# Kernel optimization log

Measured on AMD Instinct MI355X. Metric: run time of the kernel, lower is better.

Reference implementation:

```python
import jax, jax.numpy as jnp
import numpy as np

B, S, D = 2, 2048, 512
H, HD = 8, 64  # num_heads, head_size; all_head_size = H*HD = 512


def setup_inputs() -> dict:
    key = jax.random.key(0)
    ks = jax.random.split(key, 11)
    sc = 0.02
    return {
        "query": jax.random.normal(ks[0], (B, S, D), jnp.float32),
        "key": jax.random.normal(ks[1], (B, S, D), jnp.float32),
        "value": jax.random.normal(ks[2], (B, S, D), jnp.float32),
        "Wq": jax.random.normal(ks[3], (D, H * HD), jnp.float32) * sc,
        "bq": jnp.zeros((H * HD,), jnp.float32),
        "Wk": jax.random.normal(ks[4], (D, H * HD), jnp.float32) * sc,
        "bk": jnp.zeros((H * HD,), jnp.float32),
        "Wv": jax.random.normal(ks[5], (D, H * HD), jnp.float32) * sc,
        "bv": jnp.zeros((H * HD,), jnp.float32),
        "Wo": jax.random.normal(ks[6], (H * HD, D), jnp.float32) * sc,
        "bo": jnp.zeros((D,), jnp.float32),
    }


def _split_heads(x):
    b, s, _ = x.shape
    return x.reshape(b, s, H, HD).transpose(0, 2, 1, 3)  # [B,H,S,HD]


def reference(query, key, value, Wq, bq, Wk, bk, Wv, bv, Wo, bo):
    q = _split_heads(query @ Wq + bq)
    k = _split_heads(key @ Wk + bk)
    v = _split_heads(value @ Wv + bv)
    scores = jnp.einsum("bhqd,bhkd->bhqk", q, k) / jnp.sqrt(jnp.asarray(HD, q.dtype))
    probs = jax.nn.softmax(scores, axis=-1)  # dropout rate 0.0, inference
    ctx = jnp.einsum("bhqk,bhkd->bhqd", probs, v)
    ctx = ctx.transpose(0, 2, 1, 3).reshape(query.shape[0], -1, H * HD)
    return ctx @ Wo + bo
```

## Files before the change

kernel.cpp:

```cpp
#include <hip/hip_runtime.h>
#include <math.h>

#define BATCH 2
#define SEQ 2048
#define DMODEL 512
#define NH 8
#define HDIM 64
#define MTOT (BATCH * SEQ)
#define QSIZE (BATCH * NH * SEQ * HDIM)
#define WSIZE (DMODEL * DMODEL)

typedef __attribute__((ext_vector_type(8))) short bf16x8;
typedef __attribute__((ext_vector_type(4))) float f32x4;

__device__ inline unsigned short f2bf(float f) {
    union { float f; unsigned u; } v; v.f = f;
    unsigned u = v.u;
    u += 0x7fffu + ((u >> 16) & 1u);
    return (unsigned short)(u >> 16);
}
__device__ inline unsigned pack2(float lo, float hi) {
    unsigned r;
    asm("v_cvt_pk_bf16_f32 %0, %1, %2" : "=v"(r) : "v"(lo), "v"(hi));
    return r;
}

#define LSTR 72

#define WS_Q   ((size_t)0)
#define WS_K   ((size_t)QSIZE)
#define WS_V   (2 * (size_t)QSIZE)
#define WS_CTX (3 * (size_t)QSIZE)
#define WS_WT  (4 * (size_t)QSIZE)
#define WS_ABF (4 * (size_t)QSIZE + 4 * (size_t)WSIZE)

__global__ __launch_bounds__(256) void wt_prep_kernel(
    const float* __restrict__ Wq, const float* __restrict__ Wk,
    const float* __restrict__ Wv, const float* __restrict__ Wo,
    unsigned short* __restrict__ wt)
{
    const int z = blockIdx.z;
    const float* W = (z == 0) ? Wq : (z == 1) ? Wk : (z == 2) ? Wv : Wo;
    unsigned short* Wt = wt + (size_t)z * WSIZE;

    __shared__ float T[32][33];
    const int tid = threadIdx.x;
    const int k0 = blockIdx.x * 32, n0 = blockIdx.y * 32;

    {
        int r = tid >> 3, c = (tid & 7) * 4;
        float4 v = *(const float4*)&W[(size_t)(k0 + r) * DMODEL + n0 + c];
        T[r][c + 0] = v.x; T[r][c + 1] = v.y; T[r][c + 2] = v.z; T[r][c + 3] = v.w;
    }
    __syncthreads();
    {
        int n = tid >> 3, c = (tid & 7) * 4;
        uint2 o;
        o.x = pack2(T[c + 0][n], T[c + 1][n]);
        o.y = pack2(T[c + 2][n], T[c + 3][n]);
        *(uint2*)&Wt[(size_t)(n0 + n) * DMODEL + k0 + c] = o;
    }
}

__global__ __launch_bounds__(256) void inp_prep_kernel(
    const float* __restrict__ qin, const float* __restrict__ kin,
    const float* __restrict__ vin, unsigned short* __restrict__ abf)
{
    const int z = blockIdx.y;
    const float* src = (z == 0) ? qin : (z == 1) ? kin : vin;
    unsigned short* dst = abf + (size_t)z * QSIZE;

    const size_t i = ((size_t)blockIdx.x * 256 + threadIdx.x) * 8;
    float4 f0 = *(const float4*)(src + i);
    float4 f1 = *(const float4*)(src + i + 4);
    uint4 o;
    o.x = pack2(f0.x, f0.y); o.y = pack2(f0.z, f0.w);
    o.z = pack2(f1.x, f1.y); o.w = pack2(f1.z, f1.w);
    *(uint4*)(dst + i) = o;
}

__global__ __launch_bounds__(256) void qkv_mfma_kernel(
    unsigned short* __restrict__ ws,
    const float* __restrict__ bq, const float* __restrict__ bk,
    const float* __restrict__ bv)
{
    const int which = blockIdx.z;
    const unsigned short* A  = ws + WS_ABF + (size_t)which * QSIZE;
    const unsigned short* Wt = ws + WS_WT + (size_t)which * WSIZE;
    const float* bias = (which == 0) ? bq : (which == 1) ? bk : bv;
    unsigned short* out = ws + (size_t)which * QSIZE;

    __shared__ __align__(16) short As[128][LSTR];
    __shared__ __align__(16) short Bs[128][LSTR];

    const int tid = threadIdx.x;
    const int lane = tid & 63, wave = tid >> 6;
    const int lrow = lane & 15, quad = lane >> 4;
    const int m0 = blockIdx.y * 128, n0 = blockIdx.x * 128;

    const int sr = tid >> 1;
    const int sh = (tid & 1) * 32;

    f32x4 acc[2][8];
    #pragma unroll
    for (int i = 0; i < 2; ++i)
        #pragma unroll
        for (int n = 0; n < 8; ++n) acc[i][n] = f32x4{0.f, 0.f, 0.f, 0.f};

    for (int k0 = 0; k0 < DMODEL; k0 += 64) {
        __syncthreads();
        {
            const unsigned short* ap = A + (size_t)(m0 + sr) * DMODEL + k0 + sh;
            uint4 a0 = *(const uint4*)(ap + 0),  a1 = *(const uint4*)(ap + 8);
            uint4 a2 = *(const uint4*)(ap + 16), a3 = *(const uint4*)(ap + 24);
            *(uint4*)&As[sr][sh + 0]  = a0;
            *(uint4*)&As[sr][sh + 8]  = a1;
            *(uint4*)&As[sr][sh + 16] = a2;
            *(uint4*)&As[sr][sh + 24] = a3;
        }
        {
            const unsigned short* wp = Wt + (size_t)(n0 + sr) * DMODEL + k0 + sh;
            uint4 b0 = *(const uint4*)(wp + 0),  b1 = *(const uint4*)(wp + 8);
            uint4 b2 = *(const uint4*)(wp + 16), b3 = *(const uint4*)(wp + 24);
            *(uint4*)&Bs[sr][sh + 0]  = b0;
            *(uint4*)&Bs[sr][sh + 8]  = b1;
            *(uint4*)&Bs[sr][sh + 16] = b2;
            *(uint4*)&Bs[sr][sh + 24] = b3;
        }
        __syncthreads();
        #pragma unroll
        for (int s = 0; s < 2; ++s) {
            bf16x8 af[2];
            #pragma unroll
            for (int i = 0; i < 2; ++i)
                af[i] = *(const bf16x8*)&As[wave * 32 + i * 16 + lrow][s * 32 + quad * 8];
            #pragma unroll
            for (int n = 0; n < 8; ++n) {
                bf16x8 bf = *(const bf16x8*)&Bs[n * 16 + lrow][s * 32 + quad * 8];
                acc[0][n] = __builtin_amdgcn_mfma_f32_16x16x32_bf16(af[0], bf, acc[0][n], 0, 0, 0);
                acc[1][n] = __builtin_amdgcn_mfma_f32_16x16x32_bf16(af[1], bf, acc[1][n], 0, 0, 0);
            }
        }
    }

    if (which < 2) {
        const float scale = (which == 0) ? 0.125f : 1.0f;
        #pragma unroll
        for (int n = 0; n < 8; ++n) {
            const int col = n0 + n * 16 + lrow;
            const int h_ = col >> 6, hd_ = col & 63;
            const float bv_ = bias[col];
            #pragma unroll
            for (int i = 0; i < 2; ++i) {
                #pragma unroll
                for (int r = 0; r < 4; ++r) {
                    const int m = m0 + wave * 32 + i * 16 + quad * 4 + r;
                    const int b_ = m >> 11, s_ = m & (SEQ - 1);
                    const float v = (acc[i][n][r] + bv_) * scale;
                    out[((size_t)((b_ * NH + h_) * SEQ + s_)) * HDIM + hd_] = f2bf(v);
                }
            }
        }
    } else {
        #pragma unroll
        for (int n = 0; n < 8; ++n) {
            const int col = n0 + n * 16 + lrow;
            const int h_ = col >> 6, hd_ = col & 63;
            const float bv_ = bias[col];
            #pragma unroll
            for (int i = 0; i < 2; ++i) {
                const int m = m0 + wave * 32 + i * 16 + quad * 4;
                const int b_ = m >> 11, s_ = m & (SEQ - 1);
                uint2 o;
                o.x = pack2(acc[i][n][0] + bv_, acc[i][n][1] + bv_);
                o.y = pack2(acc[i][n][2] + bv_, acc[i][n][3] + bv_);
                *(uint2*)&out[((size_t)((b_ * NH + h_) * HDIM + hd_)) * SEQ + s_] = o;
            }
        }
    }
}

#define HSEQ (SEQ / 2)
#define NT   (HSEQ / 64)
#define OSTR 68

__global__ __launch_bounds__(512) void attn_mfma_kernel(
    const unsigned short* __restrict__ ws, unsigned short* __restrict__ ctx)
{
    const unsigned short* Q = ws + WS_Q;
    const unsigned short* K = ws + WS_K;
    const unsigned short* V = ws + WS_V;

    __shared__ __align__(16) short Ks[2][2][64][LSTR];
    __shared__ __align__(16) short Vt[2][2][64][LSTR];

    const int lin = blockIdx.x + 16 * blockIdx.y;
    const int bh  = (lin & 7) + 8 * (lin >> 8);
    const int q0  = ((lin >> 3) & 31) * 64;

    const int tid = threadIdx.x;
    const int lane = tid & 63, wave = tid >> 6;
    const int half = wave >> 2, w4 = wave & 3;
    const int lrow = lane & 15, quad = lane >> 4;
    const size_t base = (size_t)bh * SEQ * HDIM;

    const unsigned short* qrow = Q + base + (size_t)(q0 + w4 * 16 + lrow) * HDIM;
    const bf16x8 qb0 = *(const bf16x8*)(qrow + quad * 8);
    const bf16x8 qb1 = *(const bf16x8*)(qrow + 32 + quad * 8);

    float m_prev = -1e30f, l_run = 0.f;
    f32x4 oacc[4];
    #pragma unroll
    for (int n = 0; n < 4; ++n) oacc[n] = f32x4{0.f, 0.f, 0.f, 0.f};

    const int t  = tid & 255;
    const int kr = t >> 2;
    const int kc = (t & 3) * 16;
    const int n_ = t & 3;
    const int c0 = ((n_ >= 2) ? 32 : 0) + (n_ & 1) * 4;
    const int ktbase = half * HSEQ;

    const unsigned short* kptr = K + base + (size_t)(ktbase + kr) * HDIM + kc;
    const unsigned short* vptr = V + base + (size_t)kr * SEQ + ktbase + kc;

    uint4 kA, kB, vA, vB;
#define LOADT(TI) do { \
        const unsigned short* kp = kptr + (size_t)(TI) * 64 * HDIM; \
        const unsigned short* vp = vptr + (TI) * 64; \
        kA = *(const uint4*)kp; kB = *(const uint4*)(kp + 8); \
        vA = *(const uint4*)vp; vB = *(const uint4*)(vp + 8); \
    } while (0)
#define WRITET(BUF) do { \
        *(uint4*)&Ks[half][BUF][kr][kc]     = kA; \
        *(uint4*)&Ks[half][BUF][kr][kc + 8] = kB; \
        uint2 w0; w0.x = vA.x; w0.y = vA.y; \
        uint2 w1; w1.x = vA.z; w1.y = vA.w; \
        uint2 w2; w2.x = vB.x; w2.y = vB.y; \
        uint2 w3; w3.x = vB.z; w3.y = vB.w; \
        *(uint2*)&Vt[half][BUF][kr][c0]      = w0; \
        *(uint2*)&Vt[half][BUF][kr][c0 + 8]  = w1; \
        *(uint2*)&Vt[half][BUF][kr][c0 + 16] = w2; \
        *(uint2*)&Vt[half][BUF][kr][c0 + 24] = w3; \
    } while (0)

    LOADT(0);
    WRITET(0);
    LOADT(1);

    #pragma unroll 2
    for (int ti = 0; ti < NT; ++ti) {
        const int cur = ti & 1;
        __syncthreads();

        f32x4 st[4];
        __builtin_amdgcn_s_setprio(1);
        #pragma unroll
        for (int n = 0; n < 4; ++n) {
            bf16x8 ka0 = *(const bf16x8*)&Ks[half][cur][n * 16 + lrow][quad * 8];
            bf16x8 ka1 = *(const bf16x8*)&Ks[half][cur][n * 16 + lrow][32 + quad * 8];
            f32x4 z = f32x4{0.f, 0.f, 0.f, 0.f};
            z = __builtin_amdgcn_mfma_f32_16x16x32_bf16(ka0, qb0, z, 0, 0, 0);
            z = __builtin_amdgcn_mfma_f32_16x16x32_bf16(ka1, qb1, z, 0, 0, 0);
            st[n] = z;
        }
        __builtin_amdgcn_s_setprio(0);

        float tmax = st[0][0];
        #pragma unroll
        for (int n = 0; n < 4; ++n)
            #pragma unroll
            for (int r = 0; r < 4; ++r) tmax = fmaxf(tmax, st[n][r]);
        tmax = fmaxf(tmax, __shfl_xor(tmax, 16));
        tmax = fmaxf(tmax, __shfl_xor(tmax, 32));

        if (!__all(tmax <= m_prev + 8.f)) {
            const float mnew = fmaxf(m_prev, tmax);
            const float alpha = __expf(m_prev - mnew);
            l_run *= alpha;
            #pragma unroll
            for (int n = 0; n < 4; ++n) {
                oacc[n][0] *= alpha; oacc[n][1] *= alpha;
                oacc[n][2] *= alpha; oacc[n][3] *= alpha;
            }
            m_prev = mnew;
        }

        float p[4][4];
        float tsum = 0.f;
        #pragma unroll
        for (int n = 0; n < 4; ++n)
            #pragma unroll
            for (int r = 0; r < 4; ++r) {
                p[n][r] = __expf(st[n][r] - m_prev);
                tsum += p[n][r];
            }
        tsum += __shfl_xor(tsum, 16);
        tsum += __shfl_xor(tsum, 32);
        l_run += tsum;

        union { unsigned w[4]; bf16x8 v; } U0, U1;
        U0.w[0] = pack2(p[0][0], p[0][1]); U0.w[1] = pack2(p[0][2], p[0][3]);
        U0.w[2] = pack2(p[1][0], p[1][1]); U0.w[3] = pack2(p[1][2], p[1][3]);
        U1.w[0] = pack2(p[2][0], p[2][1]); U1.w[1] = pack2(p[2][2], p[2][3]);
        U1.w[2] = pack2(p[3][0], p[3][1]); U1.w[3] = pack2(p[3][2], p[3][3]);

        __builtin_amdgcn_s_setprio(1);
        #pragma unroll
        for (int n = 0; n < 4; ++n) {
            bf16x8 va0 = *(const bf16x8*)&Vt[half][cur][n * 16 + lrow][quad * 8];
            bf16x8 va1 = *(const bf16x8*)&Vt[half][cur][n * 16 + lrow][32 + quad * 8];
            oacc[n] = __builtin_amdgcn_mfma_f32_16x16x32_bf16(va0, U0.v, oacc[n], 0, 0, 0);
            oacc[n] = __builtin_amdgcn_mfma_f32_16x16x32_bf16(va1, U1.v, oacc[n], 0, 0, 0);
        }
        __builtin_amdgcn_s_setprio(0);

        if (ti < NT - 1) WRITET(cur ^ 1);
        if (ti < NT - 2) LOADT(ti + 2);
    }
#undef LOADT
#undef WRITET

    __syncthreads();
    float* Obuf = (float*)&Ks[0][0][0][0];
    float* Mbuf = (float*)&Vt[0][0][0][0];

    if (half == 1) {
        float* ob = Obuf + (size_t)w4 * (16 * OSTR) + (size_t)lrow * OSTR;
        #pragma unroll
        for (int n = 0; n < 4; ++n)
            *(f32x4*)&ob[n * 16 + quad * 4] = oacc[n];
        if (quad == 0) {
            Mbuf[w4 * 16 + lrow]      = m_prev;
            Mbuf[64 + w4 * 16 + lrow] = l_run;
        }
    }
    __syncthreads();
    if (half == 0) {
        const float m1 = Mbuf[w4 * 16 + lrow];
        const float l1 = Mbuf[64 + w4 * 16 + lrow];
        const float M  = fmaxf(m_prev, m1);
        const float a0 = __expf(m_prev - M), a1 = __expf(m1 - M);
        const float inv = 1.f / (l_run * a0 + l1 * a1);
        const float s0 = a0 * inv, s1 = a1 * inv;
        const float* ob = Obuf + (size_t)w4 * (16 * OSTR) + (size_t)lrow * OSTR;

        const int b_ = bh >> 3, h_ = bh & 7;
        const int qg = q0 + w4 * 16 + lrow;
        unsigned short* crow = ctx + ((size_t)(b_ * SEQ + qg)) * DMODEL + h_ * HDIM;
        #pragma unroll
        for (int n = 0; n < 4; ++n) {
            f32x4 o1 = *(const f32x4*)&ob[n * 16 + quad * 4];
            uint2 o;
            o.x = pack2(oacc[n][0] * s0 + o1[0] * s1, oacc[n][1] * s0 + o1[1] * s1);
            o.y = pack2(oacc[n][2] * s0 + o1[2] * s1, oacc[n][3] * s0 + o1[3] * s1);
            *(uint2*)&crow[n * 16 + quad * 4] = o;
        }
    }
}

__global__ __launch_bounds__(256) void out_proj_mfma_kernel(
    const unsigned short* __restrict__ ws, const float* __restrict__ bo,
    float* __restrict__ out)
{
    const unsigned short* ctx = ws + WS_CTX;
    const unsigned short* Wt  = ws + WS_WT + 3 * (size_t)WSIZE;

    __shared__ __align__(16) short As[128][LSTR];
    __shared__ __align__(16) short Bs[64][LSTR];

    const int tid = threadIdx.x;
    const int lane = tid & 63, wave = tid >> 6;
    const int lrow = lane & 15, quad = lane >> 4;
    const int m0 = blockIdx.y * 128, n0 = blockIdx.x * 64;

    const int sr = tid >> 1, sh = (tid & 1) * 32;
    const int br = tid >> 2, bqr = (tid & 3) * 16;

    f32x4 acc[2][4];
    #pragma unroll
    for (int i = 0; i < 2; ++i)
        #pragma unroll
        for (int n = 0; n < 4; ++n) acc[i][n] = f32x4{0.f, 0.f, 0.f, 0.f};

    for (int k0 = 0; k0 < DMODEL; k0 += 64) {
        __syncthreads();
        {
            const unsigned short* ap = ctx + (size_t)(m0 + sr) * DMODEL + k0 + sh;
            uint4 c0 = *(const uint4*)(ap + 0),  c1 = *(const uint4*)(ap + 8);
            uint4 c2 = *(const uint4*)(ap + 16), c3 = *(const uint4*)(ap + 24);
            *(uint4*)&As[sr][sh + 0]  = c0;
            *(uint4*)&As[sr][sh + 8]  = c1;
            *(uint4*)&As[sr][sh + 16] = c2;
            *(uint4*)&As[sr][sh + 24] = c3;
        }
        {
            const unsigned short* wp = Wt + (size_t)(n0 + br) * DMODEL + k0 + bqr;
            uint4 b0 = *(const uint4*)wp;
            uint4 b1 = *(const uint4*)(wp + 8);
            *(uint4*)&Bs[br][bqr]     = b0;
            *(uint4*)&Bs[br][bqr + 8] = b1;
        }
        __syncthreads();
        #pragma unroll
        for (int s = 0; s < 2; ++s) {
            bf16x8 af[2];
            #pragma unroll
            for (int i = 0; i < 2; ++i)
                af[i] = *(const bf16x8*)&As[wave * 32 + i * 16 + lrow][s * 32 + quad * 8];
            #pragma unroll
            for (int n = 0; n < 4; ++n) {
                bf16x8 bf = *(const bf16x8*)&Bs[n * 16 + lrow][s * 32 + quad * 8];
                acc[0][n] = __builtin_amdgcn_mfma_f32_16x16x32_bf16(af[0], bf, acc[0][n], 0, 0, 0);
                acc[1][n] = __builtin_amdgcn_mfma_f32_16x16x32_bf16(af[1], bf, acc[1][n], 0, 0, 0);
            }
        }
    }

    #pragma unroll
    for (int n = 0; n < 4; ++n) {
        const int col = n0 + n * 16 + lrow;
        const float bv_ = bo[col];
        #pragma unroll
        for (int i = 0; i < 2; ++i) {
            #pragma unroll
            for (int r = 0; r < 4; ++r) {
                const int m = m0 + wave * 32 + i * 16 + quad * 4 + r;
                out[(size_t)m * DMODEL + col] = acc[i][n][r] + bv_;
            }
        }
    }
}

extern "C" void kernel_launch(void* const* d_in, const int* in_sizes, int n_in,
                              void* d_out, int out_size, void* d_ws, size_t ws_size,
                              hipStream_t stream)
{
    const float* qin = (const float*)d_in[0];
    const float* kin = (const float*)d_in[1];
    const float* vin = (const float*)d_in[2];
    const float* Wq  = (const float*)d_in[3];
    const float* bq  = (const float*)d_in[4];
    const float* Wk  = (const float*)d_in[5];
    const float* bk  = (const float*)d_in[6];
    const float* Wv  = (const float*)d_in[7];
    const float* bv  = (const float*)d_in[8];
    const float* Wo  = (const float*)d_in[9];
    const float* bo  = (const float*)d_in[10];

    unsigned short* ws = (unsigned short*)d_ws;
    float* out = (float*)d_out;

    dim3 gw(DMODEL / 32, DMODEL / 32, 4);
    wt_prep_kernel<<<gw, 256, 0, stream>>>(Wq, Wk, Wv, Wo, ws + WS_WT);

    dim3 gi(QSIZE / (256 * 8), 3);
    inp_prep_kernel<<<gi, 256, 0, stream>>>(qin, kin, vin, ws + WS_ABF);

    dim3 gp(DMODEL / 128, MTOT / 128, 3);
    qkv_mfma_kernel<<<gp, 256, 0, stream>>>(ws, bq, bk, bv);

    dim3 ga(BATCH * NH, SEQ / 64);
    attn_mfma_kernel<<<ga, 512, 0, stream>>>(ws, ws + WS_CTX);

    dim3 go(DMODEL / 64, MTOT / 128);
    out_proj_mfma_kernel<<<go, 256, 0, stream>>>(ws, bo, out);
}
```

Baseline: 147.7 us.

## Fuse input bf16 conversion into QKV GEMM, double-buffer weights, use exp2 softmax

The separate fp32-to-bf16 input prep kernel is removed, and the QKV GEMM now loads fp32 activations straight from global memory into registers, converting them in place. Both projection GEMMs drop the A-tile shared-memory staging and double-buffer the B tile, so each k-step needs one barrier instead of two. Attention folds log2(e) into the Q scale so softmax can use exp2f, raises the lazy-rescale threshold, and does the row-sum shuffle reduction once at the end instead of every tile. The cost is uncoalesced, per-lane global reads of A that are reused from registers rather than shared memory, plus a looser rescale bound that could affect accuracy.

```diff
diff --git a/kernel.cpp b/kernel.cpp
--- a/kernel.cpp
+++ b/kernel.cpp
@@ -32,7 +32,8 @@
 #define WS_V   (2 * (size_t)QSIZE)
 #define WS_CTX (3 * (size_t)QSIZE)
 #define WS_WT  (4 * (size_t)QSIZE)
-#define WS_ABF (4 * (size_t)QSIZE + 4 * (size_t)WSIZE)
+
+#define QSCALE 0.1803368801111204f
 
 __global__ __launch_bounds__(256) void wt_prep_kernel(
     const float* __restrict__ Wq, const float* __restrict__ Wk,
@@ -62,44 +63,31 @@
     }
 }
 
-__global__ __launch_bounds__(256) void inp_prep_kernel(
-    const float* __restrict__ qin, const float* __restrict__ kin,
-    const float* __restrict__ vin, unsigned short* __restrict__ abf)
-{
-    const int z = blockIdx.y;
-    const float* src = (z == 0) ? qin : (z == 1) ? kin : vin;
-    unsigned short* dst = abf + (size_t)z * QSIZE;
-
-    const size_t i = ((size_t)blockIdx.x * 256 + threadIdx.x) * 8;
-    float4 f0 = *(const float4*)(src + i);
-    float4 f1 = *(const float4*)(src + i + 4);
-    uint4 o;
-    o.x = pack2(f0.x, f0.y); o.y = pack2(f0.z, f0.w);
-    o.z = pack2(f1.x, f1.y); o.w = pack2(f1.z, f1.w);
-    *(uint4*)(dst + i) = o;
-}
-
 __global__ __launch_bounds__(256) void qkv_mfma_kernel(
     unsigned short* __restrict__ ws,
+    const float* __restrict__ qin, const float* __restrict__ kin,
+    const float* __restrict__ vin,
     const float* __restrict__ bq, const float* __restrict__ bk,
     const float* __restrict__ bv)
 {
     const int which = blockIdx.z;
-    const unsigned short* A  = ws + WS_ABF + (size_t)which * QSIZE;
+    const float* A = (which == 0) ? qin : (which == 1) ? kin : vin;
     const unsigned short* Wt = ws + WS_WT + (size_t)which * WSIZE;
     const float* bias = (which == 0) ? bq : (which == 1) ? bk : bv;
     unsigned short* out = ws + (size_t)which * QSIZE;
 
-    __shared__ __align__(16) short As[128][LSTR];
-    __shared__ __align__(16) short Bs[128][LSTR];
+    __shared__ __align__(16) short Bs[2][128][LSTR];
 
     const int tid = threadIdx.x;
     const int lane = tid & 63, wave = tid >> 6;
     const int lrow = lane & 15, quad = lane >> 4;
     const int m0 = blockIdx.y * 128, n0 = blockIdx.x * 128;
 
-    const int sr = tid >> 1;
-    const int sh = (tid & 1) * 32;
+    const int sr = tid >> 1, sh = (tid & 1) * 32;
+    const unsigned short* wp0 = Wt + (size_t)(n0 + sr) * DMODEL + sh;
+
+    const float* arow0 = A + (size_t)(m0 + wave * 32 + lrow) * DMODEL;
+    const float* arow1 = arow0 + 16 * DMODEL;
 
     f32x4 acc[2][8];
     #pragma unroll
@@ -107,44 +95,59 @@
         #pragma unroll
         for (int n = 0; n < 8; ++n) acc[i][n] = f32x4{0.f, 0.f, 0.f, 0.f};
 
-    for (int k0 = 0; k0 < DMODEL; k0 += 64) {
+    uint4 b0, b1, b2, b3;
+#define LOADB(K0) do { const unsigned short* wp = wp0 + (K0); \
+        b0 = *(const uint4*)(wp + 0);  b1 = *(const uint4*)(wp + 8); \
+        b2 = *(const uint4*)(wp + 16); b3 = *(const uint4*)(wp + 24); } while (0)
+#define WRITEB(BUF) do { \
+        *(uint4*)&Bs[BUF][sr][sh + 0]  = b0; *(uint4*)&Bs[BUF][sr][sh + 8]  = b1; \
+        *(uint4*)&Bs[BUF][sr][sh + 16] = b2; *(uint4*)&Bs[BUF][sr][sh + 24] = b3; } while (0)
+
+    LOADB(0);
+    WRITEB(0);
+    LOADB(64);
+
+    #pragma unroll
+    for (int kk = 0; kk < 8; ++kk) {
+        const int k0 = kk * 64, cur = kk & 1;
         __syncthreads();
-        {
-            const unsigned short* ap = A + (size_t)(m0 + sr) * DMODEL + k0 + sh;
-            uint4 a0 = *(const uint4*)(ap + 0),  a1 = *(const uint4*)(ap + 8);
-            uint4 a2 = *(const uint4*)(ap + 16), a3 = *(const uint4*)(ap + 24);
-            *(uint4*)&As[sr][sh + 0]  = a0;
-            *(uint4*)&As[sr][sh + 8]  = a1;
-            *(uint4*)&As[sr][sh + 16] = a2;
-            *(uint4*)&As[sr][sh + 24] = a3;
-        }
-        {
-            const unsigned short* wp = Wt + (size_t)(n0 + sr) * DMODEL + k0 + sh;
-            uint4 b0 = *(const uint4*)(wp + 0),  b1 = *(const uint4*)(wp + 8);
-            uint4 b2 = *(const uint4*)(wp + 16), b3 = *(const uint4*)(wp + 24);
-            *(uint4*)&Bs[sr][sh + 0]  = b0;
-            *(uint4*)&Bs[sr][sh + 8]  = b1;
-            *(uint4*)&Bs[sr][sh + 16] = b2;
-            *(uint4*)&Bs[sr][sh + 24] = b3;
-        }
-        __syncthreads();
+        __builtin_amdgcn_s_setprio(1);
         #pragma unroll
         for (int s = 0; s < 2; ++s) {
+            const int cb = k0 + s * 32 + quad * 8;
             bf16x8 af[2];
-            #pragma unroll
-            for (int i = 0; i < 2; ++i)
-                af[i] = *(const bf16x8*)&As[wave * 32 + i * 16 + lrow][s * 32 + quad * 8];
+            {
+                float4 f0 = *(const float4*)(arow0 + cb);
+                float4 f1 = *(const float4*)(arow0 + cb + 4);
+                union { unsigned w[4]; bf16x8 v; } U;
+                U.w[0] = pack2(f0.x, f0.y); U.w[1] = pack2(f0.z, f0.w);
+                U.w[2] = pack2(f1.x, f1.y); U.w[3] = pack2(f1.z, f1.w);
+                af[0] = U.v;
+            }
+            {
+                float4 f0 = *(const float4*)(arow1 + cb);
+                float4 f1 = *(const float4*)(arow1 + cb + 4);
+                union { unsigned w[4]; bf16x8 v; } U;
+                U.w[0] = pack2(f0.x, f0.y); U.w[1] = pack2(f0.z, f0.w);
+                U.w[2] = pack2(f1.x, f1.y); U.w[3] = pack2(f1.z, f1.w);
+                af[1] = U.v;
+            }
             #pragma unroll
             for (int n = 0; n < 8; ++n) {
-                bf16x8 bf = *(const bf16x8*)&Bs[n * 16 + lrow][s * 32 + quad * 8];
-                acc[0][n] = __builtin_amdgcn_mfma_f32_16x16x32_bf16(af[0], bf, acc[0][n], 0, 0, 0);
-                acc[1][n] = __builtin_amdgcn_mfma_f32_16x16x32_bf16(af[1], bf, acc[1][n], 0, 0, 0);
-            }
-        }
-    }
+                bf16x8 bfv = *(const bf16x8*)&Bs[cur][n * 16 + lrow][s * 32 + quad * 8];
+                acc[0][n] = __builtin_amdgcn_mfma_f32_16x16x32_bf16(af[0], bfv, acc[0][n], 0, 0, 0);
+                acc[1][n] = __builtin_amdgcn_mfma_f32_16x16x32_bf16(af[1], bfv, acc[1][n], 0, 0, 0);
+            }
+        }
+        __builtin_amdgcn_s_setprio(0);
+        if (kk < 7) WRITEB(cur ^ 1);
+        if (kk < 6) LOADB(k0 + 128);
+    }
+#undef LOADB
+#undef WRITEB
 
     if (which < 2) {
-        const float scale = (which == 0) ? 0.125f : 1.0f;
+        const float scale = (which == 0) ? QSCALE : 1.0f;
         #pragma unroll
         for (int n = 0; n < 8; ++n) {
             const int col = n0 + n * 16 + lrow;
@@ -183,6 +186,7 @@
 #define HSEQ (SEQ / 2)
 #define NT   (HSEQ / 64)
 #define OSTR 68
+#define THR2 11.0f
 
 __global__ __launch_bounds__(512) void attn_mfma_kernel(
     const unsigned short* __restrict__ ws, unsigned short* __restrict__ ctx)
@@ -265,17 +269,17 @@
         }
         __builtin_amdgcn_s_setprio(0);
 
-        float tmax = st[0][0];
-        #pragma unroll
-        for (int n = 0; n < 4; ++n)
-            #pragma unroll
-            for (int r = 0; r < 4; ++r) tmax = fmaxf(tmax, st[n][r]);
+        float t0 = fmaxf(fmaxf(st[0][0], st[0][1]), fmaxf(st[0][2], st[0][3]));
+        float t1 = fmaxf(fmaxf(st[1][0], st[1][1]), fmaxf(st[1][2], st[1][3]));
+        float t2 = fmaxf(fmaxf(st[2][0], st[2][1]), fmaxf(st[2][2], st[2][3]));
+        float t3 = fmaxf(fmaxf(st[3][0], st[3][1]), fmaxf(st[3][2], st[3][3]));
+        float tmax = fmaxf(fmaxf(t0, t1), fmaxf(t2, t3));
         tmax = fmaxf(tmax, __shfl_xor(tmax, 16));
         tmax = fmaxf(tmax, __shfl_xor(tmax, 32));
 
-        if (!__all(tmax <= m_prev + 8.f)) {
+        if (!__all(tmax <= m_prev + THR2)) {
             const float mnew = fmaxf(m_prev, tmax);
-            const float alpha = __expf(m_prev - mnew);
+            const float alpha = exp2f(m_prev - mnew);
             l_run *= alpha;
             #pragma unroll
             for (int n = 0; n < 4; ++n) {
@@ -291,11 +295,9 @@
         for (int n = 0; n < 4; ++n)
             #pragma unroll
             for (int r = 0; r < 4; ++r) {
-                p[n][r] = __expf(st[n][r] - m_prev);
+                p[n][r] = exp2f(st[n][r] - m_prev);
                 tsum += p[n][r];
             }
-        tsum += __shfl_xor(tsum, 16);
-        tsum += __shfl_xor(tsum, 32);
         l_run += tsum;
 
         union { unsigned w[4]; bf16x8 v; } U0, U1;
@@ -320,6 +322,9 @@
 #undef LOADT
 #undef WRITET
 
+    l_run += __shfl_xor(l_run, 16);
+    l_run += __shfl_xor(l_run, 32);
+
     __syncthreads();
     float* Obuf = (float*)&Ks[0][0][0][0];
     float* Mbuf = (float*)&Vt[0][0][0][0];
@@ -339,7 +344,7 @@
         const float m1 = Mbuf[w4 * 16 + lrow];
         const float l1 = Mbuf[64 + w4 * 16 + lrow];
         const float M  = fmaxf(m_prev, m1);
-        const float a0 = __expf(m_prev - M), a1 = __expf(m1 - M);
+        const float a0 = exp2f(m_prev - M), a1 = exp2f(m1 - M);
         const float inv = 1.f / (l_run * a0 + l1 * a1);
         const float s0 = a0 * inv, s1 = a1 * inv;
         const float* ob = Obuf + (size_t)w4 * (16 * OSTR) + (size_t)lrow * OSTR;
@@ -365,16 +370,18 @@
     const unsigned short* ctx = ws + WS_CTX;
     const unsigned short* Wt  = ws + WS_WT + 3 * (size_t)WSIZE;
 
-    __shared__ __align__(16) short As[128][LSTR];
-    __shared__ __align__(16) short Bs[64][LSTR];
+    __shared__ __align__(16) short Bs[2][64][LSTR];
 
     const int tid = threadIdx.x;
     const int lane = tid & 63, wave = tid >> 6;
     const int lrow = lane & 15, quad = lane >> 4;
     const int m0 = blockIdx.y * 128, n0 = blockIdx.x * 64;
 
-    const int sr = tid >> 1, sh = (tid & 1) * 32;
-    const int br = tid >> 2, bqr = (tid & 3) * 16;
+    const int br = tid >> 2, bc = (tid & 3) * 16;
+    const unsigned short* wp0 = Wt + (size_t)(n0 + br) * DMODEL + bc;
+
+    const unsigned short* arow0 = ctx + (size_t)(m0 + wave * 32 + lrow) * DMODEL;
+    const unsigned short* arow1 = arow0 + 16 * DMODEL;
 
     f32x4 acc[2][4];
     #pragma unroll
@@ -382,39 +389,40 @@
         #pragma unroll
         for (int n = 0; n < 4; ++n) acc[i][n] = f32x4{0.f, 0.f, 0.f, 0.f};
 
-    for (int k0 = 0; k0 < DMODEL; k0 += 64) {
+    uint4 b0, b1;
+#define LOADB(K0) do { const unsigned short* wp = wp0 + (K0); \
+        b0 = *(const uint4*)(wp + 0); b1 = *(const uint4*)(wp + 8); } while (0)
+#define WRITEB(BUF) do { \
+        *(uint4*)&Bs[BUF][br][bc]     = b0; \
+        *(uint4*)&Bs[BUF][br][bc + 8] = b1; } while (0)
+
+    LOADB(0);
+    WRITEB(0);
+    LOADB(64);
+
+    #pragma unroll
+    for (int kk = 0; kk < 8; ++kk) {
+        const int k0 = kk * 64, cur = kk & 1;
         __syncthreads();
-        {
-            const unsigned short* ap = ctx + (size_t)(m0 + sr) * DMODEL + k0 + sh;
-            uint4 c0 = *(const uint4*)(ap + 0),  c1 = *(const uint4*)(ap + 8);
-            uint4 c2 = *(const uint4*)(ap + 16), c3 = *(const uint4*)(ap + 24);
-            *(uint4*)&As[sr][sh + 0]  = c0;
-            *(uint4*)&As[sr][sh + 8]  = c1;
-            *(uint4*)&As[sr][sh + 16] = c2;
-            *(uint4*)&As[sr][sh + 24] = c3;
-        }
-        {
-            const unsigned short* wp = Wt + (size_t)(n0 + br) * DMODEL + k0 + bqr;
-            uint4 b0 = *(const uint4*)wp;
-            uint4 b1 = *(const uint4*)(wp + 8);
-            *(uint4*)&Bs[br][bqr]     = b0;
-            *(uint4*)&Bs[br][bqr + 8] = b1;
-        }
-        __syncthreads();
+        __builtin_amdgcn_s_setprio(1);
         #pragma unroll
         for (int s = 0; s < 2; ++s) {
-            bf16x8 af[2];
-            #pragma unroll
-            for (int i = 0; i < 2; ++i)
-                af[i] = *(const bf16x8*)&As[wave * 32 + i * 16 + lrow][s * 32 + quad * 8];
+            const int cb = k0 + s * 32 + quad * 8;
+            bf16x8 af0 = *(const bf16x8*)(arow0 + cb);
+            bf16x8 af1 = *(const bf16x8*)(arow1 + cb);
             #pragma unroll
             for (int n = 0; n < 4; ++n) {
-                bf16x8 bf = *(const bf16x8*)&Bs[n * 16 + lrow][s * 32 + quad * 8];
-                acc[0][n] = __builtin_amdgcn_mfma_f32_16x16x32_bf16(af[0], bf, acc[0][n], 0, 0, 0);
-                acc[1][n] = __builtin_amdgcn_mfma_f32_16x16x32_bf16(af[1], bf, acc[1][n], 0, 0, 0);
-            }
-        }
-    }
+                bf16x8 bfv = *(const bf16x8*)&Bs[cur][n * 16 + lrow][s * 32 + quad * 8];
+                acc[0][n] = __builtin_amdgcn_mfma_f32_16x16x32_bf16(af0, bfv, acc[0][n], 0, 0, 0);
+                acc[1][n] = __builtin_amdgcn_mfma_f32_16x16x32_bf16(af1, bfv, acc[1][n], 0, 0, 0);
+            }
+        }
+        __builtin_amdgcn_s_setprio(0);
+        if (kk < 7) WRITEB(cur ^ 1);
+        if (kk < 6) LOADB(k0 + 128);
+    }
+#undef LOADB
+#undef WRITEB
 
     #pragma unroll
     for (int n = 0; n < 4; ++n) {
@@ -453,11 +461,8 @@
     dim3 gw(DMODEL / 32, DMODEL / 32, 4);
     wt_prep_kernel<<<gw, 256, 0, stream>>>(Wq, Wk, Wv, Wo, ws + WS_WT);
 
-    dim3 gi(QSIZE / (256 * 8), 3);
-    inp_prep_kernel<<<gi, 256, 0, stream>>>(qin, kin, vin, ws + WS_ABF);
-
     dim3 gp(DMODEL / 128, MTOT / 128, 3);
-    qkv_mfma_kernel<<<gp, 256, 0, stream>>>(ws, bq, bk, bv);
+    qkv_mfma_kernel<<<gp, 256, 0, stream>>>(ws, qin, kin, vin, bq, bk, bv);
 
     dim3 ga(BATCH * NH, SEQ / 64);
     attn_mfma_kernel<<<ga, 512, 0, stream>>>(ws, ws + WS_CTX);
```

New measurement: 156.1 us. 5.7% more time.

## Merge prep kernels, prefetch GEMM tiles, and use exp2 softmax with deferred sums

Applied to the files above, without the earlier changes.

Folds the weight-transpose and input-conversion kernels into one launch, removing a kernel launch and its tail. Both projection GEMMs now load the next K tile into registers while MFMAs run on the current tile, and raise wave priority during the MFMA section. The attention softmax moves to base 2: Q is prescaled by log2(e)/8 so exp2f can replace __expf, and the rescale threshold is widened to match. The cross-lane row-sum shuffles now run once after the loop instead of every tile. The costs are higher register pressure from the prefetch buffers and one more branch in the merged prep kernel.

```diff
diff --git a/kernel.cpp b/kernel.cpp
--- a/kernel.cpp
+++ b/kernel.cpp
@@ -34,49 +34,49 @@
 #define WS_WT  (4 * (size_t)QSIZE)
 #define WS_ABF (4 * (size_t)QSIZE + 4 * (size_t)WSIZE)
 
-__global__ __launch_bounds__(256) void wt_prep_kernel(
+#define QSCALE 0.1803368801111204f
+
+__global__ __launch_bounds__(256) void prep_kernel(
     const float* __restrict__ Wq, const float* __restrict__ Wk,
     const float* __restrict__ Wv, const float* __restrict__ Wo,
-    unsigned short* __restrict__ wt)
+    const float* __restrict__ qin, const float* __restrict__ kin,
+    const float* __restrict__ vin, unsigned short* __restrict__ ws)
 {
-    const int z = blockIdx.z;
-    const float* W = (z == 0) ? Wq : (z == 1) ? Wk : (z == 2) ? Wv : Wo;
-    unsigned short* Wt = wt + (size_t)z * WSIZE;
-
     __shared__ float T[32][33];
+    const int bid = blockIdx.x;
     const int tid = threadIdx.x;
-    const int k0 = blockIdx.x * 32, n0 = blockIdx.y * 32;
-
-    {
-        int r = tid >> 3, c = (tid & 7) * 4;
-        float4 v = *(const float4*)&W[(size_t)(k0 + r) * DMODEL + n0 + c];
-        T[r][c + 0] = v.x; T[r][c + 1] = v.y; T[r][c + 2] = v.z; T[r][c + 3] = v.w;
-    }
-    __syncthreads();
-    {
-        int n = tid >> 3, c = (tid & 7) * 4;
-        uint2 o;
-        o.x = pack2(T[c + 0][n], T[c + 1][n]);
-        o.y = pack2(T[c + 2][n], T[c + 3][n]);
-        *(uint2*)&Wt[(size_t)(n0 + n) * DMODEL + k0 + c] = o;
-    }
-}
-
-__global__ __launch_bounds__(256) void inp_prep_kernel(
-    const float* __restrict__ qin, const float* __restrict__ kin,
-    const float* __restrict__ vin, unsigned short* __restrict__ abf)
-{
-    const int z = blockIdx.y;
-    const float* src = (z == 0) ? qin : (z == 1) ? kin : vin;
-    unsigned short* dst = abf + (size_t)z * QSIZE;
-
-    const size_t i = ((size_t)blockIdx.x * 256 + threadIdx.x) * 8;
-    float4 f0 = *(const float4*)(src + i);
-    float4 f1 = *(const float4*)(src + i + 4);
-    uint4 o;
-    o.x = pack2(f0.x, f0.y); o.y = pack2(f0.z, f0.w);
-    o.z = pack2(f1.x, f1.y); o.w = pack2(f1.z, f1.w);
-    *(uint4*)(dst + i) = o;
+
+    if (bid < 1024) {
+        const int z = bid >> 8, rem = bid & 255;
+        const float* W = (z == 0) ? Wq : (z == 1) ? Wk : (z == 2) ? Wv : Wo;
+        unsigned short* Wt = ws + WS_WT + (size_t)z * WSIZE;
+        const int k0 = (rem & 15) * 32, n0 = (rem >> 4) * 32;
+        {
+            int r = tid >> 3, c = (tid & 7) * 4;
+            float4 v = *(const float4*)&W[(size_t)(k0 + r) * DMODEL + n0 + c];
+            T[r][c + 0] = v.x; T[r][c + 1] = v.y; T[r][c + 2] = v.z; T[r][c + 3] = v.w;
+        }
+        __syncthreads();
+        {
+            int n = tid >> 3, c = (tid & 7) * 4;
+            uint2 o;
+            o.x = pack2(T[c + 0][n], T[c + 1][n]);
+            o.y = pack2(T[c + 2][n], T[c + 3][n]);
+            *(uint2*)&Wt[(size_t)(n0 + n) * DMODEL + k0 + c] = o;
+        }
+    } else {
+        const int idx = bid - 1024;
+        const int z = idx >> 10, blk = idx & 1023;
+        const float* src = (z == 0) ? qin : (z == 1) ? kin : vin;
+        unsigned short* dst = ws + WS_ABF + (size_t)z * QSIZE;
+        const size_t i = ((size_t)blk * 256 + tid) * 8;
+        float4 f0 = *(const float4*)(src + i);
+        float4 f1 = *(const float4*)(src + i + 4);
+        uint4 o;
+        o.x = pack2(f0.x, f0.y); o.y = pack2(f0.z, f0.w);
+        o.z = pack2(f1.x, f1.y); o.w = pack2(f1.z, f1.w);
+        *(uint4*)(dst + i) = o;
+    }
 }
 
 __global__ __launch_bounds__(256) void qkv_mfma_kernel(
@@ -100,6 +100,8 @@
 
     const int sr = tid >> 1;
     const int sh = (tid & 1) * 32;
+    const unsigned short* ap0 = A  + (size_t)(m0 + sr) * DMODEL + sh;
+    const unsigned short* wp0 = Wt + (size_t)(n0 + sr) * DMODEL + sh;
 
     f32x4 acc[2][8];
     #pragma unroll
@@ -107,27 +109,30 @@
         #pragma unroll
         for (int n = 0; n < 8; ++n) acc[i][n] = f32x4{0.f, 0.f, 0.f, 0.f};
 
-    for (int k0 = 0; k0 < DMODEL; k0 += 64) {
-        __syncthreads();
-        {
-            const unsigned short* ap = A + (size_t)(m0 + sr) * DMODEL + k0 + sh;
-            uint4 a0 = *(const uint4*)(ap + 0),  a1 = *(const uint4*)(ap + 8);
-            uint4 a2 = *(const uint4*)(ap + 16), a3 = *(const uint4*)(ap + 24);
-            *(uint4*)&As[sr][sh + 0]  = a0;
-            *(uint4*)&As[sr][sh + 8]  = a1;
-            *(uint4*)&As[sr][sh + 16] = a2;
-            *(uint4*)&As[sr][sh + 24] = a3;
-        }
-        {
-            const unsigned short* wp = Wt + (size_t)(n0 + sr) * DMODEL + k0 + sh;
-            uint4 b0 = *(const uint4*)(wp + 0),  b1 = *(const uint4*)(wp + 8);
-            uint4 b2 = *(const uint4*)(wp + 16), b3 = *(const uint4*)(wp + 24);
-            *(uint4*)&Bs[sr][sh + 0]  = b0;
-            *(uint4*)&Bs[sr][sh + 8]  = b1;
-            *(uint4*)&Bs[sr][sh + 16] = b2;
-            *(uint4*)&Bs[sr][sh + 24] = b3;
-        }
-        __syncthreads();
+    uint4 a0, a1, a2, a3, b0, b1, b2, b3;
+#define LOADS(K0) do { \
+        const unsigned short* ap = ap0 + (K0); \
+        const unsigned short* wp = wp0 + (K0); \
+        a0 = *(const uint4*)(ap + 0);  a1 = *(const uint4*)(ap + 8); \
+        a2 = *(const uint4*)(ap + 16); a3 = *(const uint4*)(ap + 24); \
+        b0 = *(const uint4*)(wp + 0);  b1 = *(const uint4*)(wp + 8); \
+        b2 = *(const uint4*)(wp + 16); b3 = *(const uint4*)(wp + 24); } while (0)
+#define WRITES() do { \
+        *(uint4*)&As[sr][sh + 0]  = a0; *(uint4*)&As[sr][sh + 8]  = a1; \
+        *(uint4*)&As[sr][sh + 16] = a2; *(uint4*)&As[sr][sh + 24] = a3; \
+        *(uint4*)&Bs[sr][sh + 0]  = b0; *(uint4*)&Bs[sr][sh + 8]  = b1; \
+        *(uint4*)&Bs[sr][sh + 16] = b2; *(uint4*)&Bs[sr][sh + 24] = b3; } while (0)
+
+    LOADS(0);
+
+    #pragma unroll
+    for (int kk = 0; kk < 8; ++kk) {
+        const int k0 = kk * 64;
+        __syncthreads();
+        WRITES();
+        __syncthreads();
+        if (kk < 7) LOADS(k0 + 64);
+        __builtin_amdgcn_s_setprio(1);
         #pragma unroll
         for (int s = 0; s < 2; ++s) {
             bf16x8 af[2];
@@ -136,15 +141,18 @@
                 af[i] = *(const bf16x8*)&As[wave * 32 + i * 16 + lrow][s * 32 + quad * 8];
             #pragma unroll
             for (int n = 0; n < 8; ++n) {
-                bf16x8 bf = *(const bf16x8*)&Bs[n * 16 + lrow][s * 32 + quad * 8];
-                acc[0][n] = __builtin_amdgcn_mfma_f32_16x16x32_bf16(af[0], bf, acc[0][n], 0, 0, 0);
-                acc[1][n] = __builtin_amdgcn_mfma_f32_16x16x32_bf16(af[1], bf, acc[1][n], 0, 0, 0);
-            }
-        }
-    }
+                bf16x8 bfv = *(const bf16x8*)&Bs[n * 16 + lrow][s * 32 + quad * 8];
+                acc[0][n] = __builtin_amdgcn_mfma_f32_16x16x32_bf16(af[0], bfv, acc[0][n], 0, 0, 0);
+                acc[1][n] = __builtin_amdgcn_mfma_f32_16x16x32_bf16(af[1], bfv, acc[1][n], 0, 0, 0);
+            }
+        }
+        __builtin_amdgcn_s_setprio(0);
+    }
+#undef LOADS
+#undef WRITES
 
     if (which < 2) {
-        const float scale = (which == 0) ? 0.125f : 1.0f;
+        const float scale = (which == 0) ? QSCALE : 1.0f;
         #pragma unroll
         for (int n = 0; n < 8; ++n) {
             const int col = n0 + n * 16 + lrow;
@@ -183,6 +191,7 @@
 #define HSEQ (SEQ / 2)
 #define NT   (HSEQ / 64)
 #define OSTR 68
+#define THR2 11.0f
 
 __global__ __launch_bounds__(512) void attn_mfma_kernel(
     const unsigned short* __restrict__ ws, unsigned short* __restrict__ ctx)
@@ -265,17 +274,17 @@
         }
         __builtin_amdgcn_s_setprio(0);
 
-        float tmax = st[0][0];
-        #pragma unroll
-        for (int n = 0; n < 4; ++n)
-            #pragma unroll
-            for (int r = 0; r < 4; ++r) tmax = fmaxf(tmax, st[n][r]);
+        float t0 = fmaxf(fmaxf(st[0][0], st[0][1]), fmaxf(st[0][2], st[0][3]));
+        float t1 = fmaxf(fmaxf(st[1][0], st[1][1]), fmaxf(st[1][2], st[1][3]));
+        float t2 = fmaxf(fmaxf(st[2][0], st[2][1]), fmaxf(st[2][2], st[2][3]));
+        float t3 = fmaxf(fmaxf(st[3][0], st[3][1]), fmaxf(st[3][2], st[3][3]));
+        float tmax = fmaxf(fmaxf(t0, t1), fmaxf(t2, t3));
         tmax = fmaxf(tmax, __shfl_xor(tmax, 16));
         tmax = fmaxf(tmax, __shfl_xor(tmax, 32));
 
-        if (!__all(tmax <= m_prev + 8.f)) {
+        if (!__all(tmax <= m_prev + THR2)) {
             const float mnew = fmaxf(m_prev, tmax);
-            const float alpha = __expf(m_prev - mnew);
+            const float alpha = exp2f(m_prev - mnew);
             l_run *= alpha;
             #pragma unroll
             for (int n = 0; n < 4; ++n) {
@@ -291,11 +300,9 @@
         for (int n = 0; n < 4; ++n)
             #pragma unroll
             for (int r = 0; r < 4; ++r) {
-                p[n][r] = __expf(st[n][r] - m_prev);
+                p[n][r] = exp2f(st[n][r] - m_prev);
                 tsum += p[n][r];
             }
-        tsum += __shfl_xor(tsum, 16);
-        tsum += __shfl_xor(tsum, 32);
         l_run += tsum;
 
         union { unsigned w[4]; bf16x8 v; } U0, U1;
@@ -320,6 +327,9 @@
 #undef LOADT
 #undef WRITET
 
+    l_run += __shfl_xor(l_run, 16);
+    l_run += __shfl_xor(l_run, 32);
+
     __syncthreads();
     float* Obuf = (float*)&Ks[0][0][0][0];
     float* Mbuf = (float*)&Vt[0][0][0][0];
@@ -339,7 +349,7 @@
         const float m1 = Mbuf[w4 * 16 + lrow];
         const float l1 = Mbuf[64 + w4 * 16 + lrow];
         const float M  = fmaxf(m_prev, m1);
-        const float a0 = __expf(m_prev - M), a1 = __expf(m1 - M);
+        const float a0 = exp2f(m_prev - M), a1 = exp2f(m1 - M);
         const float inv = 1.f / (l_run * a0 + l1 * a1);
         const float s0 = a0 * inv, s1 = a1 * inv;
         const float* ob = Obuf + (size_t)w4 * (16 * OSTR) + (size_t)lrow * OSTR;
@@ -375,6 +385,8 @@
 
     const int sr = tid >> 1, sh = (tid & 1) * 32;
     const int br = tid >> 2, bqr = (tid & 3) * 16;
+    const unsigned short* ap0 = ctx + (size_t)(m0 + sr) * DMODEL + sh;
+    const unsigned short* wp0 = Wt + (size_t)(n0 + br) * DMODEL + bqr;
 
     f32x4 acc[2][4];
     #pragma unroll
@@ -382,25 +394,28 @@
         #pragma unroll
         for (int n = 0; n < 4; ++n) acc[i][n] = f32x4{0.f, 0.f, 0.f, 0.f};
 
-    for (int k0 = 0; k0 < DMODEL; k0 += 64) {
-        __syncthreads();
-        {
-            const unsigned short* ap = ctx + (size_t)(m0 + sr) * DMODEL + k0 + sh;
-            uint4 c0 = *(const uint4*)(ap + 0),  c1 = *(const uint4*)(ap + 8);
-            uint4 c2 = *(const uint4*)(ap + 16), c3 = *(const uint4*)(ap + 24);
-            *(uint4*)&As[sr][sh + 0]  = c0;
-            *(uint4*)&As[sr][sh + 8]  = c1;
-            *(uint4*)&As[sr][sh + 16] = c2;
-            *(uint4*)&As[sr][sh + 24] = c3;
-        }
-        {
-            const unsigned short* wp = Wt + (size_t)(n0 + br) * DMODEL + k0 + bqr;
-            uint4 b0 = *(const uint4*)wp;
-            uint4 b1 = *(const uint4*)(wp + 8);
-            *(uint4*)&Bs[br][bqr]     = b0;
-            *(uint4*)&Bs[br][bqr + 8] = b1;
-        }
-        __syncthreads();
+    uint4 a0, a1, a2, a3, b0, b1;
+#define LOADS(K0) do { \
+        const unsigned short* ap = ap0 + (K0); \
+        const unsigned short* wp = wp0 + (K0); \
+        a0 = *(const uint4*)(ap + 0);  a1 = *(const uint4*)(ap + 8); \
+        a2 = *(const uint4*)(ap + 16); a3 = *(const uint4*)(ap + 24); \
+        b0 = *(const uint4*)wp; b1 = *(const uint4*)(wp + 8); } while (0)
+#define WRITES() do { \
+        *(uint4*)&As[sr][sh + 0]  = a0; *(uint4*)&As[sr][sh + 8]  = a1; \
+        *(uint4*)&As[sr][sh + 16] = a2; *(uint4*)&As[sr][sh + 24] = a3; \
+        *(uint4*)&Bs[br][bqr]     = b0; *(uint4*)&Bs[br][bqr + 8] = b1; } while (0)
+
+    LOADS(0);
+
+    #pragma unroll
+    for (int kk = 0; kk < 8; ++kk) {
+        const int k0 = kk * 64;
+        __syncthreads();
+        WRITES();
+        __syncthreads();
+        if (kk < 7) LOADS(k0 + 64);
+        __builtin_amdgcn_s_setprio(1);
         #pragma unroll
         for (int s = 0; s < 2; ++s) {
             bf16x8 af[2];
@@ -409,12 +424,15 @@
                 af[i] = *(const bf16x8*)&As[wave * 32 + i * 16 + lrow][s * 32 + quad * 8];
             #pragma unroll
             for (int n = 0; n < 4; ++n) {
-                bf16x8 bf = *(const bf16x8*)&Bs[n * 16 + lrow][s * 32 + quad * 8];
-                acc[0][n] = __builtin_amdgcn_mfma_f32_16x16x32_bf16(af[0], bf, acc[0][n], 0, 0, 0);
-                acc[1][n] = __builtin_amdgcn_mfma_f32_16x16x32_bf16(af[1], bf, acc[1][n], 0, 0, 0);
-            }
-        }
-    }
+                bf16x8 bfv = *(const bf16x8*)&Bs[n * 16 + lrow][s * 32 + quad * 8];
+                acc[0][n] = __builtin_amdgcn_mfma_f32_16x16x32_bf16(af[0], bfv, acc[0][n], 0, 0, 0);
+                acc[1][n] = __builtin_amdgcn_mfma_f32_16x16x32_bf16(af[1], bfv, acc[1][n], 0, 0, 0);
+            }
+        }
+        __builtin_amdgcn_s_setprio(0);
+    }
+#undef LOADS
+#undef WRITES
 
     #pragma unroll
     for (int n = 0; n < 4; ++n) {
@@ -450,11 +468,7 @@
     unsigned short* ws = (unsigned short*)d_ws;
     float* out = (float*)d_out;
 
-    dim3 gw(DMODEL / 32, DMODEL / 32, 4);
-    wt_prep_kernel<<<gw, 256, 0, stream>>>(Wq, Wk, Wv, Wo, ws + WS_WT);
-
-    dim3 gi(QSIZE / (256 * 8), 3);
-    inp_prep_kernel<<<gi, 256, 0, stream>>>(qin, kin, vin, ws + WS_ABF);
+    prep_kernel<<<4096, 256, 0, stream>>>(Wq, Wk, Wv, Wo, qin, kin, vin, ws);
 
     dim3 gp(DMODEL / 128, MTOT / 128, 3);
     qkv_mfma_kernel<<<gp, 256, 0, stream>>>(ws, bq, bk, bv);
```

Result: no change. 148.7 us (median of 3 runs) (+0.7%).
